# Performance work log

Hardware: AMD Instinct MI355X
Metric: run time of the kernel (lower is better)

The kernel has to match this reference:

```python
import jax, jax.numpy as jnp
import numpy as np

N_E = 16384
E_DIM = 256


def setup_inputs() -> dict:
    key = jax.random.key(0)
    k1, k2 = jax.random.split(key)
    z = jax.random.normal(k1, (16, E_DIM, 32, 32), dtype=jnp.float32)
    # nn.Embedding init: uniform(-1/n_e, 1/n_e)
    embedding_weight = jax.random.uniform(
        k2, (N_E, E_DIM), dtype=jnp.float32, minval=-1.0 / N_E, maxval=1.0 / N_E
    )
    return {"z": z, "embedding_weight": embedding_weight}


def reference(z, embedding_weight):
    # b c h w -> b h w c, flatten to (N, e_dim)
    zf = jnp.transpose(z, (0, 2, 3, 1)).reshape(-1, E_DIM)  # [N, d]
    # squared euclidean distances: ||z||^2 + ||e||^2 - 2 z.e^T
    d = (
        jnp.sum(zf ** 2, axis=1, keepdims=True)          # [N, 1]
        + jnp.sum(embedding_weight ** 2, axis=1)         # [n_e]
        - 2.0 * jnp.einsum("bd,nd->bn", zf, embedding_weight)  # [N, n_e]
    )
    min_encoding_indices = jnp.argmin(d, axis=1)  # [N] int
    return min_encoding_indices
```

## Files before the change

kernel.cpp:

```cpp
#include <hip/hip_runtime.h>

#define EDIM 256
#define NROW 16384
#define NCODE 16384
#define NBN 128
#define MARGIN 2.0e-4f

typedef _Float16 f16x8 __attribute__((ext_vector_type(8)));
typedef _Float16 f16x4 __attribute__((ext_vector_type(4)));
typedef float f32x4 __attribute__((ext_vector_type(4)));

__device__ __forceinline__ void gll16(const void* g, void* l) {
  __builtin_amdgcn_global_load_lds((const __attribute__((address_space(1))) void*)g,
                                   (__attribute__((address_space(3))) void*)l, 16, 0, 0);
}
__device__ __forceinline__ void gll4(const void* g, void* l) {
  __builtin_amdgcn_global_load_lds((const __attribute__((address_space(1))) void*)g,
                                   (__attribute__((address_space(3))) void*)l, 4, 0, 0);
}

__global__ __launch_bounds__(256) void k_prep_e(const float* __restrict__ e,
                                                float* __restrict__ es,
                                                _Float16* __restrict__ Eh) {
  const int row = blockIdx.x * 4 + (threadIdx.x >> 6);
  const int lane = threadIdx.x & 63;
  float4 v = *(const float4*)&e[row * EDIM + lane * 4];
  f16x4 h;
  h[0] = (_Float16)(v.x * 1024.0f);
  h[1] = (_Float16)(v.y * 1024.0f);
  h[2] = (_Float16)(v.z * 1024.0f);
  h[3] = (_Float16)(v.w * 1024.0f);
  *(f16x4*)&Eh[row * EDIM + lane * 4] = h;
  double s = (double)v.x * v.x + (double)v.y * v.y + (double)v.z * v.z + (double)v.w * v.w;
#pragma unroll
  for (int off = 32; off > 0; off >>= 1) s += __shfl_down(s, off, 64);
  if (lane == 0) es[row] = (float)s;
}

__global__ __launch_bounds__(256) void k_es(const float* __restrict__ e,
                                            float* __restrict__ es) {
  const int row = blockIdx.x * 4 + (threadIdx.x >> 6);
  const int lane = threadIdx.x & 63;
  float4 v = *(const float4*)&e[row * EDIM + lane * 4];
  double s = (double)v.x * v.x + (double)v.y * v.y + (double)v.z * v.z + (double)v.w * v.w;
#pragma unroll
  for (int off = 32; off > 0; off >>= 1) s += __shfl_down(s, off, 64);
  if (lane == 0) es[row] = (float)s;
}

__global__ __launch_bounds__(256) void k_cvt_z(const float* __restrict__ z,
                                               _Float16* __restrict__ Zh) {
  __shared__ float zl[EDIM * 33];
  const int t = threadIdx.x;
  const int rb = blockIdx.x;
  const int bb = rb >> 5;
  const int hw0 = (rb & 31) << 5;
  const float* zbase = z + (size_t)bb * EDIM * 1024 + hw0;
#pragma unroll 4
  for (int rep = 0; rep < 32; ++rep) {
    int c = rep * 8 + (t >> 5);
    zl[c * 33 + (t & 31)] = zbase[(size_t)c * 1024 + (t & 31)];
  }
  __syncthreads();
  const int mloc = t >> 3, part = t & 7;
#pragma unroll
  for (int i = 0; i < 4; ++i) {
    int c0 = part * 32 + i * 8;
    f16x8 v;
#pragma unroll
    for (int j = 0; j < 8; ++j) v[j] = (_Float16)zl[(c0 + j) * 33 + mloc];
    *(f16x8*)&Zh[(size_t)(rb * 32 + mloc) * EDIM + c0] = v;
  }
}

__global__ __launch_bounds__(512, 8) void k_gemm(const _Float16* __restrict__ Zh,
                                                 const _Float16* __restrict__ Eh,
                                                 float* __restrict__ lmin,
                                                 uint4* __restrict__ masks) {
  __shared__ __align__(16) char smem[32768];
  char* smemA = smem;
  char* smemB = smem + 16384;

  const int tid = threadIdx.x;
  const int lane = tid & 63;
  const int wv = tid >> 6;
  const int wm = wv & 1;
  const int wn = wv >> 1;
  const int fr = lane & 15;
  const int fq = lane >> 4;
  const int swz = (fq ^ ((fr >> 1) & 3)) * 16;

  const int bid = (int)blockIdx.x;
  const int wgid = (bid & 7) * 2048 + (bid >> 3);
  const int st = wgid >> 8, wi = wgid & 255;
  const int bm = ((st & 7) << 4) | (wi & 15);
  const int bn = ((st >> 3) << 4) | (wi >> 4);

  const char* zh_b = (const char*)Zh;
  const char* eh_b = (const char*)Eh;

  const int L = tid * 16;
  const int srow = L >> 6, sp_ = (L >> 4) & 3;
  const int gsw = (sp_ ^ ((srow >> 1) & 3)) * 16;
  auto stage = [&](int buf, int s) {
    gll16(zh_b + (size_t)(bm * 128 + srow) * 512 + s * 64 + gsw, smemA + buf * 8192 + L);
    gll16(eh_b + (size_t)(bn * 128 + srow) * 512 + s * 64 + gsw, smemB + buf * 8192 + L);
  };

  f32x4 acc[4][2];
#pragma unroll
  for (int i = 0; i < 4; ++i)
#pragma unroll
    for (int j = 0; j < 2; ++j) acc[i][j] = (f32x4)0.0f;

  stage(0, 0);
  int buf = 0;
#pragma unroll 1
  for (int s = 0; s < 8; ++s) {
    if (s + 1 < 8) {
      stage(buf ^ 1, s + 1);
      asm volatile("s_waitcnt vmcnt(2)\n\ts_barrier" ::: "memory");
    } else {
      asm volatile("s_waitcnt vmcnt(0)\n\ts_barrier" ::: "memory");
    }
    const char* aB = smemA + buf * 8192;
    const char* bB = smemB + buf * 8192;
    f16x8 af[4], bf[2];
#pragma unroll
    for (int mi = 0; mi < 4; ++mi)
      af[mi] = *(const f16x8*)(aB + (wm * 64 + mi * 16 + fr) * 64 + swz);
#pragma unroll
    for (int ni = 0; ni < 2; ++ni)
      bf[ni] = *(const f16x8*)(bB + (wn * 32 + ni * 16 + fr) * 64 + swz);
    __builtin_amdgcn_s_setprio(1);
#pragma unroll
    for (int mi = 0; mi < 4; ++mi)
#pragma unroll
      for (int ni = 0; ni < 2; ++ni)
        acc[mi][ni] = __builtin_amdgcn_mfma_f32_16x16x32_f16(af[mi], bf[ni], acc[mi][ni], 0, 0, 0);
    __builtin_amdgcn_s_setprio(0);
    asm volatile("s_waitcnt lgkmcnt(0)\n\ts_barrier" ::: "memory");
    buf ^= 1;
  }

  float* rowsmax = (float*)smem;
  float* thrs = (float*)(smem + 2048);
  unsigned short* msk16 = (unsigned short*)(smem + 2560);
  const float sc = -0.001953125f;
#pragma unroll
  for (int mi = 0; mi < 4; ++mi)
#pragma unroll
    for (int r = 0; r < 4; ++r) {
      float v = fmaxf(acc[mi][0][r], acc[mi][1][r]);
#pragma unroll
      for (int off = 1; off < 16; off <<= 1) v = fmaxf(v, __shfl_xor(v, off, 64));
      if (fr == 0) rowsmax[(wm * 64 + mi * 16 + fq * 4 + r) * 4 + wn] = v;
    }
  __syncthreads();
  if (tid < 128) {
    float mx = fmaxf(fmaxf(rowsmax[tid * 4], rowsmax[tid * 4 + 1]),
                     fmaxf(rowsmax[tid * 4 + 2], rowsmax[tid * 4 + 3]));
    float rm = sc * mx;
    thrs[tid] = (rm + MARGIN) * (-512.0f);
    lmin[(size_t)bn * NROW + bm * 128 + tid] = rm;
  }
  __syncthreads();
#pragma unroll
  for (int mi = 0; mi < 4; ++mi)
#pragma unroll
    for (int r = 0; r < 4; ++r) {
      const int row = wm * 64 + mi * 16 + fq * 4 + r;
      const float th = thrs[row];
#pragma unroll
      for (int ni = 0; ni < 2; ++ni) {
        unsigned long long bal = __ballot(acc[mi][ni][r] >= th);
        if (fr == 0)
          msk16[row * 8 + wn * 2 + ni] = (unsigned short)((bal >> (fq * 16)) & 0xffffull);
      }
    }
  __syncthreads();
  if (tid < 128)
    masks[(size_t)bn * NROW + bm * 128 + tid] = *(const uint4*)&msk16[tid * 8];
}

__global__ __launch_bounds__(256) void k_rescore(const float* __restrict__ z,
                                                 const float* __restrict__ e,
                                                 const float* __restrict__ es,
                                                 const float* __restrict__ lmin,
                                                 const uint4* __restrict__ masks,
                                                 int* __restrict__ out) {
  extern __shared__ float zl[];
  float* lmin_s = zl + EDIM * 33;
  const int t = threadIdx.x;
  const int rb = (int)blockIdx.x;
  const int bb = rb >> 5;
  const int hw0 = (rb & 31) << 5;
  const int r0 = rb * 32;
  const float* zbase = z + (size_t)bb * EDIM * 1024 + hw0;
#pragma unroll 4
  for (int rep = 0; rep < 32; ++rep) {
    int c = rep * 8 + (t >> 5);
    zl[c * 33 + (t & 31)] = zbase[(size_t)c * 1024 + (t & 31)];
  }
#pragma unroll 4
  for (int rep = 0; rep < 16; ++rep) {
    int bn = rep * 8 + (t >> 5);
    lmin_s[bn * 33 + (t & 31)] = lmin[(size_t)bn * NROW + r0 + (t & 31)];
  }
  __syncthreads();

  const int r = t >> 3, q8 = t & 7, q = q8 & 3;
  const int row = r0 + r;

  double sq = 0.0;
  {
    const float* zq = zl + (q * 64) * 33 + r;
    for (int k = 0; k < 64; ++k) {
      float v = zq[k * 33];
      sq = fma((double)v, (double)v, sq);
    }
  }
  double s01 = sq + __shfl_xor(sq, 1, 64);
  double zsd = s01 + __shfl_xor(s01, 2, 64);
  const float zs = (float)zsd;

  float g = 3.402823466e+38f;
#pragma unroll
  for (int j = 0; j < 16; ++j) g = fminf(g, lmin_s[(q8 * 16 + j) * 33 + r]);
  g = fminf(g, __shfl_xor(g, 1, 64));
  g = fminf(g, __shfl_xor(g, 2, 64));
  g = fminf(g, __shfl_xor(g, 4, 64));
  const float thr = g + MARGIN;

  float bestd = 3.402823466e+38f;
  int besti = 0x7fffffff;
#pragma unroll 1
  for (int j = 0; j < 16; ++j) {
    const int bn = q8 * 16 + j;
    if (lmin_s[bn * 33 + r] <= thr) {
      uint4 mk = masks[(size_t)bn * NROW + row];
      unsigned w[4] = {mk.x, mk.y, mk.z, mk.w};
#pragma unroll 1
      for (int qq = 0; qq < 4; ++qq) {
        unsigned u = w[qq];
        while (u) {
          int b = __ffs(u) - 1;
          u &= u - 1;
          const int code = bn * 128 + qq * 32 + b;
          const float* ep = e + (size_t)code * EDIM;
          float dot = 0.0f;
          for (int k = 0; k < EDIM; k += 4) {
            float4 ev = *(const float4*)(ep + k);
            dot = fmaf(zl[(k + 0) * 33 + r], ev.x, dot);
            dot = fmaf(zl[(k + 1) * 33 + r], ev.y, dot);
            dot = fmaf(zl[(k + 2) * 33 + r], ev.z, dot);
            dot = fmaf(zl[(k + 3) * 33 + r], ev.w, dot);
          }
          float d = (zs + es[code]) - 2.0f * dot;
          if (d < bestd) {
            bestd = d;
            besti = code;
          }
        }
      }
    }
  }
#pragma unroll
  for (int off = 1; off <= 4; off <<= 1) {
    float ov = __shfl_xor(bestd, off, 64);
    int oi = __shfl_xor(besti, off, 64);
    if (ov < bestd || (ov == bestd && oi < besti)) {
      bestd = ov;
      besti = oi;
    }
  }
  if (q8 == 0) out[row] = besti;
}

__global__ __launch_bounds__(256) void k_merge(const float* __restrict__ candv,
                                               const int* __restrict__ candi,
                                               int* __restrict__ out) {
  int n = blockIdx.x * 256 + threadIdx.x;
  float v0 = candv[n], v1 = candv[NROW + n];
  int i0 = candi[n], i1 = candi[NROW + n];
  out[n] = (v1 < v0) ? i1 : i0;
}

template <int SPLIT>
__global__ __launch_bounds__(256, 2) void k_main_fb(const float* __restrict__ z,
                                                    const float* __restrict__ e,
                                                    const float* __restrict__ es,
                                                    float* __restrict__ candv,
                                                    int* __restrict__ candi,
                                                    int* __restrict__ outd) {
  extern __shared__ char smemc[];
  float* As = (float*)smemc;
  float* Bs = (float*)(smemc + 16384);
  double* zred = (double*)(smemc + 16384 + 32768);
  float* zsf = (float*)(smemc + 16384 + 32768 + 2048);
  const int tid = threadIdx.x;
  const int lane = tid & 63;
  const int wv = tid >> 6;
  const int tm = tid & 7;
  const int tn = tid >> 3;
  const int rt = (int)blockIdx.x / SPLIT;
  const int sp = (int)blockIdx.x % SPLIT;
  const int bb = rt >> 4;
  const int hw0 = (rt & 15) << 6;
  const float* zb = z + bb * (EDIM * 1024) + hw0;
  const int codeBase = sp * (NCODE / SPLIT);
  const int NSTEP = (NCODE / SPLIT) / 256 * 8;
  auto stageA = [&](int buf, int gts) {
    const int k0 = (gts & 7) * 32;
    const float* g0 = zb + (size_t)k0 * 1024 + lane;
    float* l0 = As + buf * 2048 + (wv * 8) * 64;
#pragma unroll
    for (int s = 0; s < 8; ++s) gll4(g0 + (size_t)(wv * 8 + s) * 1024, l0 + s * 64);
  };
  float4 bpre[8];
  auto loadB = [&](int gts) {
    const int ct = gts >> 3, k0 = (gts & 7) * 32;
    const float* g = e + (size_t)(codeBase + ct * 256 + tid) * 256 + k0;
#pragma unroll
    for (int s = 0; s < 8; ++s) bpre[s] = *(const float4*)(g + s * 4);
  };
  auto writeB = [&](int buf) {
    float* bw_ = Bs + buf * 8192 + tid;
#pragma unroll
    for (int s = 0; s < 8; ++s) {
      bw_[(4 * s + 0) * 256] = bpre[s].x;
      bw_[(4 * s + 1) * 256] = bpre[s].y;
      bw_[(4 * s + 2) * 256] = bpre[s].z;
      bw_[(4 * s + 3) * 256] = bpre[s].w;
    }
  };
  stageA(0, 0);
  loadB(0);
  {
    const int m = tid & 63, qt = tid >> 6;
    const float* zp = zb + (size_t)(qt * 64) * 1024 + m;
    double s = 0.0;
    for (int k = 0; k < 64; ++k) {
      float v = zp[(size_t)k * 1024];
      s = fma((double)v, (double)v, s);
    }
    zred[qt * 64 + m] = s;
  }
  writeB(0);
  __syncthreads();
  if (tid < 64) {
    double sz = (zred[tid] + zred[64 + tid]) + (zred[128 + tid] + zred[192 + tid]);
    zsf[tid] = (float)sz;
  }
  __syncthreads();
  float zsr[8];
#pragma unroll
  for (int i = 0; i < 8; ++i) zsr[i] = zsf[tm * 8 + i];
  __syncthreads();
  float bestv[8];
  int besti[8];
#pragma unroll
  for (int i = 0; i < 8; ++i) {
    bestv[i] = 3.402823466e+38f;
    besti[i] = 0;
  }
  float acc[8][8];
  int cur = 0;
#pragma unroll 1
  for (int step = 0; step < NSTEP; ++step) {
    const int kc = step & 7, ct = step >> 3;
    if (step + 1 < NSTEP) {
      stageA(cur ^ 1, step + 1);
      loadB(step + 1);
    }
    if (kc == 0) {
#pragma unroll
      for (int i = 0; i < 8; ++i)
#pragma unroll
        for (int j = 0; j < 8; ++j) acc[i][j] = 0.0f;
    }
    const float* ak = As + cur * 2048 + tm * 8;
    const float* bk = Bs + cur * 8192 + tn * 8;
#pragma unroll 4
    for (int k = 0; k < 32; ++k) {
      float4 a0 = *(const float4*)(ak + k * 64);
      float4 a1 = *(const float4*)(ak + k * 64 + 4);
      float4 b0 = *(const float4*)(bk + k * 256);
      float4 b1 = *(const float4*)(bk + k * 256 + 4);
      float av[8] = {a0.x, a0.y, a0.z, a0.w, a1.x, a1.y, a1.z, a1.w};
      float bw[8] = {b0.x, b0.y, b0.z, b0.w, b1.x, b1.y, b1.z, b1.w};
#pragma unroll
      for (int i = 0; i < 8; ++i)
#pragma unroll
        for (int j = 0; j < 8; ++j) acc[i][j] = fmaf(av[i], bw[j], acc[i][j]);
    }
    if (step + 1 < NSTEP) writeB(cur ^ 1);
    if (kc == 7) {
      const int cb = codeBase + ct * 256 + tn * 8;
#pragma unroll
      for (int j = 0; j < 8; ++j) {
        float ej = es[cb + j];
#pragma unroll
        for (int i = 0; i < 8; ++i) {
          float d = (zsr[i] + ej) - 2.0f * acc[i][j];
          if (d < bestv[i]) {
            bestv[i] = d;
            besti[i] = cb + j;
          }
        }
      }
    }
    __syncthreads();
    cur ^= 1;
  }
  float* Lv = (float*)(smemc + 16384);
  int* Li = (int*)(smemc + 16384 + 8192);
#pragma unroll
  for (int i = 0; i < 8; ++i) {
    Lv[(tm * 8 + i) * 32 + tn] = bestv[i];
    Li[(tm * 8 + i) * 32 + tn] = besti[i];
  }
  __syncthreads();
  if (tid < 64) {
    float bv = Lv[tid * 32];
    int bi = Li[tid * 32];
#pragma unroll 1
    for (int g2 = 1; g2 < 32; ++g2) {
      float v = Lv[tid * 32 + g2];
      int ii = Li[tid * 32 + g2];
      if (v < bv || (v == bv && ii < bi)) {
        bv = v;
        bi = ii;
      }
    }
    if (SPLIT == 1) outd[rt * 64 + tid] = bi;
    else {
      candv[sp * NROW + rt * 64 + tid] = bv;
      candi[sp * NROW + rt * 64 + tid] = bi;
    }
  }
}

extern "C" void kernel_launch(void* const* d_in, const int* in_sizes, int n_in,
                              void* d_out, int out_size, void* d_ws, size_t ws_size,
                              hipStream_t stream) {
  const float* z = (const float*)d_in[0];
  const float* e = (const float*)d_in[1];
  int* out = (int*)d_out;

  char* ws = (char*)d_ws;
  float* es = (float*)ws;
  const size_t off_zh = 65536;
  const size_t off_eh = off_zh + (size_t)NROW * EDIM * 2;
  const size_t off_lmin = off_eh + (size_t)NCODE * EDIM * 2;
  const size_t off_masks = off_lmin + (size_t)NROW * NBN * 4;
  const size_t need = off_masks + (size_t)NROW * NBN * 16;

  if (ws_size >= need) {
    _Float16* Zh = (_Float16*)(ws + off_zh);
    _Float16* Eh = (_Float16*)(ws + off_eh);
    float* lmin = (float*)(ws + off_lmin);
    uint4* masks = (uint4*)(ws + off_masks);
    k_prep_e<<<dim3(NCODE / 4), dim3(256), 0, stream>>>(e, es, Eh);
    k_cvt_z<<<dim3(512), dim3(256), 0, stream>>>(z, Zh);
    k_gemm<<<dim3(16384), dim3(512), 0, stream>>>(Zh, Eh, lmin, masks);
    const int rs_smem = (EDIM * 33 + NBN * 33) * 4;
    hipFuncSetAttribute(reinterpret_cast<const void*>(&k_rescore),
                        hipFuncAttributeMaxDynamicSharedMemorySize, rs_smem);
    k_rescore<<<dim3(512), dim3(256), rs_smem, stream>>>(z, e, es, lmin, masks, out);
  } else {
    k_es<<<dim3(NCODE / 4), dim3(256), 0, stream>>>(e, es);
    float* candv = (float*)(ws + 65536);
    int* candi = (int*)(ws + 65536 + 131072);
    const size_t smem = 16384 + 65536;
    if (ws_size >= 65536 + 131072 + 131072) {
      hipFuncSetAttribute(reinterpret_cast<const void*>(&k_main_fb<2>),
                          hipFuncAttributeMaxDynamicSharedMemorySize, (int)smem);
      k_main_fb<2><<<dim3(512), dim3(256), smem, stream>>>(z, e, es, candv, candi, out);
      k_merge<<<dim3(NROW / 256), dim3(256), 0, stream>>>(candv, candi, out);
    } else {
      hipFuncSetAttribute(reinterpret_cast<const void*>(&k_main_fb<1>),
                          hipFuncAttributeMaxDynamicSharedMemorySize, (int)smem);
      k_main_fb<1><<<dim3(256), dim3(256), smem, stream>>>(z, e, es, candv, candi, out);
    }
  }
}
```

Baseline: 387.6 us.

## Enlarge GEMM tile to 256x256 with 128KB LDS double-buffer and interleaved staging

The fp16 MFMA distance GEMM moves from 128x128 tiles with K-steps of 32 to 256x256 tiles with K-steps of 64. Each wave now holds 8x4 accumulator fragments, and next-stage global-to-LDS loads are spread across four sub-quadrant compute phases. A new XOR swizzle suits the 128-byte rows. The aim is higher arithmetic intensity and fewer redundant global and LDS loads per MFMA, at the cost of far more LDS (128KB dynamic), more registers, and lower occupancy (launch bounds 512,2). The epilogue is rewritten to keep the existing per-128-column lmin and mask layout, so the rescore kernel is unchanged.

```diff
diff --git a/kernel.cpp b/kernel.cpp
--- a/kernel.cpp
+++ b/kernel.cpp
@@ -73,114 +73,146 @@
   }
 }
 
-__global__ __launch_bounds__(512, 8) void k_gemm(const _Float16* __restrict__ Zh,
+__global__ __launch_bounds__(512, 2) void k_gemm(const _Float16* __restrict__ Zh,
                                                  const _Float16* __restrict__ Eh,
                                                  float* __restrict__ lmin,
                                                  uint4* __restrict__ masks) {
-  __shared__ __align__(16) char smem[32768];
-  char* smemA = smem;
-  char* smemB = smem + 16384;
+  extern __shared__ __align__(16) char smem[];
 
   const int tid = threadIdx.x;
   const int lane = tid & 63;
   const int wv = tid >> 6;
-  const int wm = wv & 1;
-  const int wn = wv >> 1;
+  const int wm = wv >> 2;
+  const int wn = wv & 3;
   const int fr = lane & 15;
   const int fq = lane >> 4;
-  const int swz = (fq ^ ((fr >> 1) & 3)) * 16;
 
   const int bid = (int)blockIdx.x;
-  const int wgid = (bid & 7) * 2048 + (bid >> 3);
-  const int st = wgid >> 8, wi = wgid & 255;
-  const int bm = ((st & 7) << 4) | (wi & 15);
-  const int bn = ((st >> 3) << 4) | (wi >> 4);
+  const int wgid = (bid & 7) * 512 + (bid >> 3);
+  const int st = wgid >> 6, wi = wgid & 63;
+  const int bm = ((st & 7) << 3) | (wi & 7);
+  const int bn = ((st >> 3) << 3) | (wi >> 3);
 
   const char* zh_b = (const char*)Zh;
   const char* eh_b = (const char*)Eh;
 
-  const int L = tid * 16;
-  const int srow = L >> 6, sp_ = (L >> 4) & 3;
-  const int gsw = (sp_ ^ ((srow >> 1) & 3)) * 16;
-  auto stage = [&](int buf, int s) {
-    gll16(zh_b + (size_t)(bm * 128 + srow) * 512 + s * 64 + gsw, smemA + buf * 8192 + L);
-    gll16(eh_b + (size_t)(bn * 128 + srow) * 512 + s * 64 + gsw, smemB + buf * 8192 + L);
+  auto stage = [&](int buf, int t, int q) {
+    const int isB = q >> 1, h = q & 1;
+    const char* src = isB ? eh_b : zh_b;
+    const int gbase = (isB ? bn : bm) * 256 + h * 128;
+    char* dst = smem + (size_t)isB * 65536 + buf * 32768 + h * 16384;
+#pragma unroll
+    for (int i = 0; i < 2; ++i) {
+      const int L = i * 8192 + tid * 16;
+      const int row = L >> 7;
+      const int p = (L >> 4) & 7;
+      const int grow = gbase + row;
+      gll16(src + (size_t)grow * 512 + (size_t)t * 128 + (((p ^ (grow & 7)) & 7) * 16),
+            dst + L);
+    }
   };
 
-  f32x4 acc[4][2];
-#pragma unroll
-  for (int i = 0; i < 4; ++i)
-#pragma unroll
-    for (int j = 0; j < 2; ++j) acc[i][j] = (f32x4)0.0f;
-
-  stage(0, 0);
+  f32x4 acc[8][4];
+#pragma unroll
+  for (int i = 0; i < 8; ++i)
+#pragma unroll
+    for (int j = 0; j < 4; ++j) acc[i][j] = (f32x4)0.0f;
+
+#pragma unroll
+  for (int q = 0; q < 4; ++q) stage(0, 0, q);
+  asm volatile("s_waitcnt vmcnt(0)\n\ts_barrier" ::: "memory");
+
   int buf = 0;
 #pragma unroll 1
-  for (int s = 0; s < 8; ++s) {
-    if (s + 1 < 8) {
-      stage(buf ^ 1, s + 1);
-      asm volatile("s_waitcnt vmcnt(2)\n\ts_barrier" ::: "memory");
-    } else {
-      asm volatile("s_waitcnt vmcnt(0)\n\ts_barrier" ::: "memory");
-    }
-    const char* aB = smemA + buf * 8192;
-    const char* bB = smemB + buf * 8192;
-    f16x8 af[4], bf[2];
-#pragma unroll
-    for (int mi = 0; mi < 4; ++mi)
-      af[mi] = *(const f16x8*)(aB + (wm * 64 + mi * 16 + fr) * 64 + swz);
-#pragma unroll
-    for (int ni = 0; ni < 2; ++ni)
-      bf[ni] = *(const f16x8*)(bB + (wn * 32 + ni * 16 + fr) * 64 + swz);
-    __builtin_amdgcn_s_setprio(1);
-#pragma unroll
-    for (int mi = 0; mi < 4; ++mi)
-#pragma unroll
-      for (int ni = 0; ni < 2; ++ni)
-        acc[mi][ni] = __builtin_amdgcn_mfma_f32_16x16x32_f16(af[mi], bf[ni], acc[mi][ni], 0, 0, 0);
-    __builtin_amdgcn_s_setprio(0);
-    asm volatile("s_waitcnt lgkmcnt(0)\n\ts_barrier" ::: "memory");
+  for (int t = 0; t < 4; ++t) {
+#pragma unroll
+    for (int q = 0; q < 4; ++q) {
+      const int qr = q >> 1, qc = q & 1;
+      const char* aT = smem + buf * 32768;
+      const char* bT = smem + 65536 + buf * 32768;
+      f16x8 af[4][2], bf[2][2];
+#pragma unroll
+      for (int mi2 = 0; mi2 < 4; ++mi2) {
+        const int row = wm * 128 + qr * 64 + mi2 * 16 + fr;
+#pragma unroll
+        for (int kk = 0; kk < 2; ++kk)
+          af[mi2][kk] = *(const f16x8*)(aT + row * 128 + (((kk * 4 + fq) ^ (row & 7)) * 16));
+      }
+#pragma unroll
+      for (int ni2 = 0; ni2 < 2; ++ni2) {
+        const int brow = wn * 64 + qc * 32 + ni2 * 16 + fr;
+#pragma unroll
+        for (int kk = 0; kk < 2; ++kk)
+          bf[ni2][kk] = *(const f16x8*)(bT + brow * 128 + (((kk * 4 + fq) ^ (brow & 7)) * 16));
+      }
+      if (t + 1 < 4) stage(buf ^ 1, t + 1, q);
+      __builtin_amdgcn_s_barrier();
+      __builtin_amdgcn_s_setprio(1);
+#pragma unroll
+      for (int kk = 0; kk < 2; ++kk)
+#pragma unroll
+        for (int mi2 = 0; mi2 < 4; ++mi2)
+#pragma unroll
+          for (int ni2 = 0; ni2 < 2; ++ni2)
+            acc[qr * 4 + mi2][qc * 2 + ni2] = __builtin_amdgcn_mfma_f32_16x16x32_f16(
+                af[mi2][kk], bf[ni2][kk], acc[qr * 4 + mi2][qc * 2 + ni2], 0, 0, 0);
+      __builtin_amdgcn_s_setprio(0);
+      if (q == 3 && t + 1 < 4) {
+        asm volatile("s_waitcnt vmcnt(0)\n\ts_barrier" ::: "memory");
+      } else {
+        __builtin_amdgcn_s_barrier();
+      }
+    }
     buf ^= 1;
   }
+  __syncthreads();
 
   float* rowsmax = (float*)smem;
-  float* thrs = (float*)(smem + 2048);
-  unsigned short* msk16 = (unsigned short*)(smem + 2560);
+  float* thrs = (float*)(smem + 4096);
+  unsigned short* msk16 = (unsigned short*)(smem + 6144);
   const float sc = -0.001953125f;
 #pragma unroll
-  for (int mi = 0; mi < 4; ++mi)
+  for (int mi = 0; mi < 8; ++mi)
 #pragma unroll
     for (int r = 0; r < 4; ++r) {
-      float v = fmaxf(acc[mi][0][r], acc[mi][1][r]);
+      float v = fmaxf(fmaxf(acc[mi][0][r], acc[mi][1][r]),
+                      fmaxf(acc[mi][2][r], acc[mi][3][r]));
 #pragma unroll
       for (int off = 1; off < 16; off <<= 1) v = fmaxf(v, __shfl_xor(v, off, 64));
-      if (fr == 0) rowsmax[(wm * 64 + mi * 16 + fq * 4 + r) * 4 + wn] = v;
-    }
-  __syncthreads();
-  if (tid < 128) {
-    float mx = fmaxf(fmaxf(rowsmax[tid * 4], rowsmax[tid * 4 + 1]),
-                     fmaxf(rowsmax[tid * 4 + 2], rowsmax[tid * 4 + 3]));
-    float rm = sc * mx;
-    thrs[tid] = (rm + MARGIN) * (-512.0f);
-    lmin[(size_t)bn * NROW + bm * 128 + tid] = rm;
-  }
-  __syncthreads();
-#pragma unroll
-  for (int mi = 0; mi < 4; ++mi)
+      if (fr == 0) {
+        const int row = wm * 128 + (mi >> 2) * 64 + (mi & 3) * 16 + fq * 4 + r;
+        rowsmax[row * 4 + wn] = v;
+      }
+    }
+  __syncthreads();
+  if (tid < 256) {
+    float lo = sc * fmaxf(rowsmax[tid * 4 + 0], rowsmax[tid * 4 + 1]);
+    float hi = sc * fmaxf(rowsmax[tid * 4 + 2], rowsmax[tid * 4 + 3]);
+    thrs[tid * 2 + 0] = (lo + MARGIN) * (-512.0f);
+    thrs[tid * 2 + 1] = (hi + MARGIN) * (-512.0f);
+    lmin[(size_t)(bn * 2 + 0) * NROW + bm * 256 + tid] = lo;
+    lmin[(size_t)(bn * 2 + 1) * NROW + bm * 256 + tid] = hi;
+  }
+  __syncthreads();
+#pragma unroll
+  for (int mi = 0; mi < 8; ++mi)
 #pragma unroll
     for (int r = 0; r < 4; ++r) {
-      const int row = wm * 64 + mi * 16 + fq * 4 + r;
-      const float th = thrs[row];
-#pragma unroll
-      for (int ni = 0; ni < 2; ++ni) {
+      const int row = wm * 128 + (mi >> 2) * 64 + (mi & 3) * 16 + fq * 4 + r;
+      const float th = thrs[row * 2 + (wn >> 1)];
+#pragma unroll
+      for (int ni = 0; ni < 4; ++ni) {
         unsigned long long bal = __ballot(acc[mi][ni][r] >= th);
         if (fr == 0)
-          msk16[row * 8 + wn * 2 + ni] = (unsigned short)((bal >> (fq * 16)) & 0xffffull);
-      }
-    }
-  __syncthreads();
-  if (tid < 128)
-    masks[(size_t)bn * NROW + bm * 128 + tid] = *(const uint4*)&msk16[tid * 8];
+          msk16[row * 16 + (wn >> 1) * 8 + (wn & 1) * 4 + ni] =
+              (unsigned short)((bal >> (fq * 16)) & 0xffffull);
+      }
+    }
+  __syncthreads();
+  if (tid < 256) {
+    masks[(size_t)(bn * 2 + 0) * NROW + bm * 256 + tid] = *(const uint4*)&msk16[tid * 16 + 0];
+    masks[(size_t)(bn * 2 + 1) * NROW + bm * 256 + tid] = *(const uint4*)&msk16[tid * 16 + 8];
+  }
 }
 
 __global__ __launch_bounds__(256) void k_rescore(const float* __restrict__ z,
@@ -463,7 +495,9 @@
     uint4* masks = (uint4*)(ws + off_masks);
     k_prep_e<<<dim3(NCODE / 4), dim3(256), 0, stream>>>(e, es, Eh);
     k_cvt_z<<<dim3(512), dim3(256), 0, stream>>>(z, Zh);
-    k_gemm<<<dim3(16384), dim3(512), 0, stream>>>(Zh, Eh, lmin, masks);
+    hipFuncSetAttribute(reinterpret_cast<const void*>(&k_gemm),
+                        hipFuncAttributeMaxDynamicSharedMemorySize, 131072);
+    k_gemm<<<dim3(4096), dim3(512), 131072, stream>>>(Zh, Eh, lmin, masks);
     const int rs_smem = (EDIM * 33 + NBN * 33) * 4;
     hipFuncSetAttribute(reinterpret_cast<const void*>(&k_rescore),
                         hipFuncAttributeMaxDynamicSharedMemorySize, rs_smem);
```

New measurement: 448.3 us. +15.7%, slower.
